# Performance work log

Hardware: AMD Instinct MI355X
Metric: run time of the kernel (lower is better)

## Reference

```python
import jax, jax.numpy as jnp
import numpy as np


def setup_inputs() -> dict:
    key = jax.random.key(0)
    k1, k2, k3 = jax.random.split(key, 3)
    B, D, C = 512, 256, 1000
    embedding = jax.random.normal(k1, (B, D), dtype=jnp.float32)
    labels = jax.random.randint(k2, (B,), 0, C, dtype=jnp.int64)
    W = jax.random.normal(k3, (C, D), dtype=jnp.float32) * 0.02
    return {"embedding": embedding, "labels": labels, "W": W}


def reference(embedding, labels, W):
    # MRL-E loss: (1/D) * sum_{k=1..D} CE(z[:, :k] @ W[:, :k].T, y)
    # Computed incrementally: logits_k = logits_{k-1} + z[:, k] outer W[:, k],
    # which is mathematically identical to recomputing the prefix matmul.
    B, D = embedding.shape
    C = W.shape[0]
    rows = jnp.arange(B)
    labels = labels.astype(jnp.int32)

    def step(logits, cols):
        z_col, w_col = cols  # [B], [C]
        logits = logits + z_col[:, None] * w_col[None, :]  # rank-1 update, [B, C]
        # stable cross-entropy: mean(logsumexp(logits) - logits[i, y_i])
        lse = jax.nn.logsumexp(logits, axis=-1)  # [B]
        lab_logit = logits[rows, labels]  # [B]
        loss_k = jnp.mean(lse - lab_logit)
        return logits, loss_k

    init = jnp.zeros((B, C), dtype=embedding.dtype)
    _, losses = jax.lax.scan(step, init, (embedding.T, W.T))  # losses: [D]
    return jnp.sum(losses) / D
```

## Files before the change

### kernel.cpp

```cpp
#include <hip/hip_runtime.h>
#include <hip/hip_bf16.h>
#include <math.h>


#define MRLE_B 512
#define MRLE_D 256
#define MRLE_C 1000
#define MRLE_CP 1024
#define MRLE_KROWS 264
#define MRLE_NT 512
#define ROWD (MRLE_CP / 2)
#define RSTR 17
#define LOG2E 1.4426950408889634f
#define LN2   0.6931471805599453f

#if __has_builtin(__builtin_amdgcn_exp2f)
#define EXP2(x) __builtin_amdgcn_exp2f(x)
#else
#define EXP2(x) __builtin_exp2f(x)
#endif

__global__ __launch_bounds__(256) void mrle_transpose(
    const float* __restrict__ W, unsigned short* __restrict__ Wtb,
    float* __restrict__ out)
{
    __shared__ float tile[64][65];
    const int c0 = blockIdx.x * 64;
    const int k0 = blockIdx.y * 64;
    const int t  = threadIdx.x;
    const int r  = t >> 2;
    const int q  = t & 3;

    if (c0 == 0 && k0 == 0 && t == 0) out[0] = 0.f;

#pragma unroll
    for (int j = 0; j < 4; ++j) {
        const int c    = c0 + r;
        const int kcol = q * 4 + j * 16;
        float4 v = make_float4(0.f, 0.f, 0.f, 0.f);
        if (c < MRLE_C) v = *(const float4*)&W[(size_t)c * MRLE_D + k0 + kcol];
        tile[r][kcol + 0] = v.x;
        tile[r][kcol + 1] = v.y;
        tile[r][kcol + 2] = v.z;
        tile[r][kcol + 3] = v.w;
    }
    __syncthreads();

#pragma unroll
    for (int j = 0; j < 4; ++j) {
        const int cc = q * 4 + j * 16;
        unsigned short hh[4];
#pragma unroll
        for (int e = 0; e < 4; ++e) {
            const float f = tile[cc + e][r] * LOG2E;
            unsigned int u = __float_as_uint(f);
            u = (u + 0x7FFFu + ((u >> 16) & 1u)) >> 16;
            hh[e] = (unsigned short)u;
        }
        *(ushort4*)&Wtb[(size_t)(k0 + r) * MRLE_CP + c0 + cc] =
            make_ushort4(hh[0], hh[1], hh[2], hh[3]);
    }
}

__global__ __launch_bounds__(MRLE_NT) void mrle_main(
    const float* __restrict__ z,
    const int* __restrict__ labels,
    const float* __restrict__ W,
    const unsigned short* __restrict__ Wtb,
    float* __restrict__ out)
{
    __shared__ float zsh[MRLE_D];
    __shared__ float red[8 * 64 * RSTR];
    __shared__ float Sw[8 * MRLE_D];
    __shared__ float wred[8];

    const int i  = blockIdx.x;
    const int t  = threadIdx.x;
    const int wv = t >> 6;
    const int l  = t & 63;

    if (t < MRLE_D) zsh[t] = z[i * MRLE_D + t];
    __syncthreads();

    const int cbase = 2 * t;
    float l0 = (cbase     < MRLE_C) ? 0.f : -INFINITY;
    float l1 = (cbase + 1 < MRLE_C) ? 0.f : -INFINITY;

    const unsigned int* Wp = (const unsigned int*)Wtb + t;

    unsigned int wbuf[8];
#pragma unroll
    for (int q = 0; q < 8; ++q) wbuf[q] = Wp[(size_t)q * ROWD];

    float* redw = red + wv * (64 * RSTR);
    float* wr = redw + l * RSTR;
    const float* rd = redw + (l & 48) * RSTR + (l & 15);

#pragma unroll 1
    for (int cb = 0; cb < 16; ++cb) {
        float r[16];
        if (cb > 0) {
#pragma unroll
            for (int u = 0; u < 16; ++u) r[u] = rd[u * RSTR];
        }

        float zq[16];
        *(float4*)&zq[0]  = *(const float4*)&zsh[cb * 16 + 0];
        *(float4*)&zq[4]  = *(const float4*)&zsh[cb * 16 + 4];
        *(float4*)&zq[8]  = *(const float4*)&zsh[cb * 16 + 8];
        *(float4*)&zq[12] = *(const float4*)&zsh[cb * 16 + 12];

#pragma unroll
        for (int kk4 = 0; kk4 < 4; ++kk4) {
            const unsigned int* qp =
                Wp + (size_t)(cb * 16 + kk4 * 4 + 10) * ROWD;
#pragma unroll
            for (int j = 0; j < 4; ++j) {
                const int kk = kk4 * 4 + j;
                const unsigned int w = wbuf[kk & 7];
                const float w0 = __uint_as_float(w << 16);
                const float w1 = __uint_as_float(w);
                l0 = fmaf(zq[kk], w0, l0);
                l1 = fmaf(zq[kk], w1, l1);
                wr[kk] = EXP2(l0) + EXP2(l1);
                wbuf[kk & 7] = qp[(j - 2) * (int)ROWD];
            }
        }

        if (cb > 0) {
            float s = 0.f;
#pragma unroll
            for (int u = 0; u < 16; ++u) s += r[u];
            s += __shfl_xor(s, 16);
            s += __shfl_xor(s, 32);
            if (l < 16) Sw[wv * MRLE_D + (cb - 1) * 16 + l] = s;
        }
    }

    {
        float s = 0.f;
#pragma unroll
        for (int u = 0; u < 16; ++u) s += rd[u * RSTR];
        s += __shfl_xor(s, 16);
        s += __shfl_xor(s, 32);
        if (l < 16) Sw[wv * MRLE_D + 15 * 16 + l] = s;
    }

    __syncthreads();

    float v = 0.f;
    if (t < MRLE_D) {
        float S = 0.f;
#pragma unroll
        for (int wq = 0; wq < 8; ++wq) S += Sw[wq * MRLE_D + t];
        const float lse = LN2 * __log2f(S);

        const int y = labels[i];
        const float lab = zsh[t] * W[(size_t)y * MRLE_D + t] *
                          (float)(MRLE_D - t);
        v = lse - lab;
    }

#pragma unroll
    for (int d = 1; d < 64; d <<= 1) v += __shfl_xor(v, d);
    if (l == 0) wred[wv] = v;
    __syncthreads();
    if (t == 0) {
        float tot = 0.f;
#pragma unroll
        for (int wq = 0; wq < 8; ++wq) tot += wred[wq];
        atomicAdd(out, tot * (1.0f / ((float)MRLE_B * (float)MRLE_D)));
    }
}

extern "C" void kernel_launch(void* const* d_in, const int* in_sizes, int n_in,
                              void* d_out, int out_size, void* d_ws, size_t ws_size,
                              hipStream_t stream) {
    const float* z      = (const float*)d_in[0];
    const int*   labels = (const int*)d_in[1];
    const float* W      = (const float*)d_in[2];
    float*       out    = (float*)d_out;

    unsigned short* Wtb = (unsigned short*)d_ws;

    mrle_transpose<<<dim3(16, 4), 256, 0, stream>>>(W, Wtb, out);
    mrle_main<<<MRLE_B, MRLE_NT, 0, stream>>>(z, labels, W, Wtb, out);
}
```

Before: 35.58 us.

## Split each batch row's k-range across two blocks to double grid parallelism

Launches two blocks per batch row, each handling half of the D prefix steps. The second block first runs the 128 leading rank-1 updates without computing exponentials so that its logits reach the right starting state, then computes the logsumexp terms for k in 128..255. Label-logit terms are computed only by the first block. This doubles the grid to fill more CUs and shortens the critical path per block, at the cost of redundant FMA and weight loads for the first half in the second block.

```diff
diff --git a/kernel.cpp b/kernel.cpp
--- a/kernel.cpp
+++ b/kernel.cpp
@@ -71,13 +71,15 @@
 {
     __shared__ float zsh[MRLE_D];
     __shared__ float red[8 * 64 * RSTR];
-    __shared__ float Sw[8 * MRLE_D];
+    __shared__ float Sw[8 * 128];
     __shared__ float wred[8];
 
-    const int i  = blockIdx.x;
-    const int t  = threadIdx.x;
-    const int wv = t >> 6;
-    const int l  = t & 63;
+    const int bid = blockIdx.x;
+    const int i   = bid >> 1;
+    const int h   = bid & 1;
+    const int t   = threadIdx.x;
+    const int wv  = t >> 6;
+    const int l   = t & 63;
 
     if (t < MRLE_D) zsh[t] = z[i * MRLE_D + t];
     __syncthreads();
@@ -96,8 +98,36 @@
     float* wr = redw + l * RSTR;
     const float* rd = redw + (l & 48) * RSTR + (l & 15);
 
+    if (h) {
 #pragma unroll 1
-    for (int cb = 0; cb < 16; ++cb) {
+        for (int cb = 0; cb < 8; ++cb) {
+            float zq[16];
+            *(float4*)&zq[0]  = *(const float4*)&zsh[cb * 16 + 0];
+            *(float4*)&zq[4]  = *(const float4*)&zsh[cb * 16 + 4];
+            *(float4*)&zq[8]  = *(const float4*)&zsh[cb * 16 + 8];
+            *(float4*)&zq[12] = *(const float4*)&zsh[cb * 16 + 12];
+#pragma unroll
+            for (int kk4 = 0; kk4 < 4; ++kk4) {
+                const unsigned int* qp =
+                    Wp + (size_t)(cb * 16 + kk4 * 4 + 10) * ROWD;
+#pragma unroll
+                for (int j = 0; j < 4; ++j) {
+                    const int kk = kk4 * 4 + j;
+                    const unsigned int w = wbuf[kk & 7];
+                    const float w0 = __uint_as_float(w << 16);
+                    const float w1 = __uint_as_float(w);
+                    l0 = fmaf(zq[kk], w0, l0);
+                    l1 = fmaf(zq[kk], w1, l1);
+                    wbuf[kk & 7] = qp[(j - 2) * (int)ROWD];
+                }
+            }
+        }
+    }
+
+    const int kst = h * 128;
+
+#pragma unroll 1
+    for (int cb = 0; cb < 8; ++cb) {
         float r[16];
         if (cb > 0) {
 #pragma unroll
@@ -105,15 +135,15 @@
         }
 
         float zq[16];
-        *(float4*)&zq[0]  = *(const float4*)&zsh[cb * 16 + 0];
-        *(float4*)&zq[4]  = *(const float4*)&zsh[cb * 16 + 4];
-        *(float4*)&zq[8]  = *(const float4*)&zsh[cb * 16 + 8];
-        *(float4*)&zq[12] = *(const float4*)&zsh[cb * 16 + 12];
+        *(float4*)&zq[0]  = *(const float4*)&zsh[kst + cb * 16 + 0];
+        *(float4*)&zq[4]  = *(const float4*)&zsh[kst + cb * 16 + 4];
+        *(float4*)&zq[8]  = *(const float4*)&zsh[kst + cb * 16 + 8];
+        *(float4*)&zq[12] = *(const float4*)&zsh[kst + cb * 16 + 12];
 
 #pragma unroll
         for (int kk4 = 0; kk4 < 4; ++kk4) {
             const unsigned int* qp =
-                Wp + (size_t)(cb * 16 + kk4 * 4 + 10) * ROWD;
+                Wp + (size_t)(kst + cb * 16 + kk4 * 4 + 10) * ROWD;
 #pragma unroll
             for (int j = 0; j < 4; ++j) {
                 const int kk = kk4 * 4 + j;
@@ -133,7 +163,7 @@
             for (int u = 0; u < 16; ++u) s += r[u];
             s += __shfl_xor(s, 16);
             s += __shfl_xor(s, 32);
-            if (l < 16) Sw[wv * MRLE_D + (cb - 1) * 16 + l] = s;
+            if (l < 16) Sw[wv * 128 + (cb - 1) * 16 + l] = s;
         }
     }
 
@@ -143,22 +173,21 @@
         for (int u = 0; u < 16; ++u) s += rd[u * RSTR];
         s += __shfl_xor(s, 16);
         s += __shfl_xor(s, 32);
-        if (l < 16) Sw[wv * MRLE_D + 15 * 16 + l] = s;
+        if (l < 16) Sw[wv * 128 + 7 * 16 + l] = s;
     }
 
     __syncthreads();
 
     float v = 0.f;
-    if (t < MRLE_D) {
+    if (t < 128) {
         float S = 0.f;
 #pragma unroll
-        for (int wq = 0; wq < 8; ++wq) S += Sw[wq * MRLE_D + t];
-        const float lse = LN2 * __log2f(S);
-
+        for (int wq = 0; wq < 8; ++wq) S += Sw[wq * 128 + t];
+        v = LN2 * __log2f(S);
+    } else if (h == 0 && t < 128 + MRLE_D) {
+        const int j = t - 128;
         const int y = labels[i];
-        const float lab = zsh[t] * W[(size_t)y * MRLE_D + t] *
-                          (float)(MRLE_D - t);
-        v = lse - lab;
+        v = -zsh[j] * W[(size_t)y * MRLE_D + j] * (float)(MRLE_D - j);
     }
 
 #pragma unroll
@@ -184,5 +213,5 @@
     unsigned short* Wtb = (unsigned short*)d_ws;
 
     mrle_transpose<<<dim3(16, 4), 256, 0, stream>>>(W, Wtb, out);
-    mrle_main<<<MRLE_B, MRLE_NT, 0, stream>>>(z, labels, W, Wtb, out);
+    mrle_main<<<MRLE_B * 2, MRLE_NT, 0, stream>>>(z, labels, W, Wtb, out);
 }
```

Measured after the change: 41.82 us. 1.18x slower.
